# Performance work log

Hardware: AMD Instinct MI355X
Metric: run time of the kernel (lower is better)

The kernel has to match this reference:

```python
import jax, jax.numpy as jnp
import numpy as np

K = 512
U = 2
TEMP_BERN = 0.67
TEMP_CAT = 0.67
EULER = 0.5772156649015329
EPS = 1e-8
UEPS = 1e-6


def setup_inputs() -> dict:
    key = jax.random.key(0)
    ks = jax.random.split(key, 3)
    B, D = 16384, 1024
    inputs = jax.random.normal(ks[0], (B, D), jnp.float32)
    # glorot-normal-ish init for mW
    mW = jax.random.normal(ks[1], (D, K * U), jnp.float32) * jnp.sqrt(2.0 / (D + K * U))
    sW = jnp.full((D, K * U), -5.0, jnp.float32)
    conc1 = jnp.full((K,), 2.0, jnp.float32)
    conc0 = jnp.full((K,), 0.5453, jnp.float32)
    t_pi = jax.random.uniform(ks[2], (D, K), jnp.float32, 4.0, 5.0)
    biases = jnp.full((K * U,), 0.1, jnp.float32)
    return {"inputs": inputs, "mW": mW, "sW": sW, "conc1": conc1,
            "conc0": conc0, "t_pi": t_pi, "biases": biases}


def _uniform(k, shape):
    return jax.random.uniform(k, shape, jnp.float32, UEPS, 1.0 - UEPS)


def reference(inputs, mW, sW, conc1, conc0, t_pi, biases):
    rk = jax.random.split(jax.random.key(42), 4)

    # --- reparameterized weights W = mW + eps * softplus(sW) ---
    sW_sp = jax.nn.softplus(sW)
    eps = jax.lax.stop_gradient(jax.random.normal(rk[0], mW.shape, jnp.float32))
    W = mW + eps * sW_sp
    kl_weights = -0.5 * jnp.mean(2.0 * sW_sp - jnp.square(mW) - jnp.square(sW_sp) + 1.0)
    layer_loss = kl_weights / 60000.0

    # --- IBP: relaxed Bernoulli sample of t_pi ([D, K]) ---
    u = _uniform(rk[1], t_pi.shape)
    logistic = jnp.log(u) - jnp.log1p(-u)
    z_sample = jax.nn.sigmoid((t_pi + logistic) / TEMP_BERN)  # bin_concrete_sample
    z = jnp.tile(z_sample, (1, U))  # [D, K*U], column order u*K+k (as in TF code)

    # Kumaraswamy stick-breaking prior: cumprod along axis 0 (TF default)
    a_sp = jax.nn.softplus(conc1)  # [K]
    b_sp = jax.nn.softplus(conc0)  # [K]
    uk = _uniform(rk[2], t_pi.shape)
    q_u = jnp.power(1.0 - jnp.power(uk, 1.0 / b_sp), 1.0 / a_sp)  # kumaraswamy_sample
    prior_pi = jnp.cumprod(q_u, axis=0)
    q = jax.nn.sigmoid(t_pi)
    kl_z = jnp.sum(q * (jnp.log(q + EPS) - jnp.log(prior_pi + EPS)))

    # KL(Kumaraswamy(a,b) || Beta(1,1)); (beta-1) series term vanishes
    kl_sticks = jnp.sum(((a_sp - 1.0) / a_sp) * (-EULER - jax.scipy.special.digamma(b_sp) - 1.0 / b_sp)
                        + jnp.log(a_sp * b_sp + EPS) - (b_sp - 1.0) / b_sp)
    layer_loss = layer_loss + kl_sticks + kl_z

    W = z * W
    out = inputs @ W + biases  # [B, K*U]

    # --- LWTA activation via Gumbel-softmax over U competitors ---
    logits = out.reshape(-1, K, U)  # [B, K, U]
    g = -jnp.log(-jnp.log(_uniform(rk[3], logits.shape)))
    xi = jax.nn.softmax((logits + g) / TEMP_CAT, axis=-1)  # concrete_sample
    out_act = (logits * xi).reshape(out.shape)
    q_xi = jax.nn.softmax(logits, axis=-1)
    kl_xi = jnp.mean(jnp.sum(q_xi * (jnp.log(q_xi + EPS) - jnp.log(1.0 / U)), axis=1))
    layer_loss = layer_loss + kl_xi

    return out_act, layer_loss
```

## Files before the change

kernel.cpp:

```cpp
#include <hip/hip_runtime.h>
#include <stdint.h>
#include <math.h>

#define B_N   16384
#define D_N   1024
#define K_N   512
#define KU_N  1024
#define EPS_F 1e-8f
#define TEMP  0.67f
#define EULERC 0.5772156649015329f

#define HEPS  524288
#define HU    262144
#define HG    8388608

typedef uint32_t u32;
typedef __attribute__((ext_vector_type(4))) float f32x4;
typedef __attribute__((ext_vector_type(4))) unsigned int u32x4;
typedef __attribute__((ext_vector_type(8))) __bf16 bf16x8;

#define TF_ROT(x, r) (((x) << (r)) | ((x) >> (32 - (r))))

__host__ __device__ static inline void threefry2x32(u32 k0, u32 k1,
                                                    u32 x0, u32 x1,
                                                    u32* o0, u32* o1) {
  u32 ks2 = k0 ^ k1 ^ 0x1BD11BDAu;
  x0 += k0; x1 += k1;
  x0 += x1; x1 = TF_ROT(x1, 13); x1 ^= x0;
  x0 += x1; x1 = TF_ROT(x1, 15); x1 ^= x0;
  x0 += x1; x1 = TF_ROT(x1, 26); x1 ^= x0;
  x0 += x1; x1 = TF_ROT(x1, 6);  x1 ^= x0;
  x0 += k1; x1 += ks2 + 1u;
  x0 += x1; x1 = TF_ROT(x1, 17); x1 ^= x0;
  x0 += x1; x1 = TF_ROT(x1, 29); x1 ^= x0;
  x0 += x1; x1 = TF_ROT(x1, 16); x1 ^= x0;
  x0 += x1; x1 = TF_ROT(x1, 24); x1 ^= x0;
  x0 += ks2; x1 += k0 + 2u;
  x0 += x1; x1 = TF_ROT(x1, 13); x1 ^= x0;
  x0 += x1; x1 = TF_ROT(x1, 15); x1 ^= x0;
  x0 += x1; x1 = TF_ROT(x1, 26); x1 ^= x0;
  x0 += x1; x1 = TF_ROT(x1, 6);  x1 ^= x0;
  x0 += k0; x1 += k1 + 3u;
  x0 += x1; x1 = TF_ROT(x1, 17); x1 ^= x0;
  x0 += x1; x1 = TF_ROT(x1, 29); x1 ^= x0;
  x0 += x1; x1 = TF_ROT(x1, 16); x1 ^= x0;
  x0 += x1; x1 = TF_ROT(x1, 24); x1 ^= x0;
  x0 += k1; x1 += ks2 + 4u;
  x0 += x1; x1 = TF_ROT(x1, 13); x1 ^= x0;
  x0 += x1; x1 = TF_ROT(x1, 15); x1 ^= x0;
  x0 += x1; x1 = TF_ROT(x1, 26); x1 ^= x0;
  x0 += x1; x1 = TF_ROT(x1, 6);  x1 ^= x0;
  x0 += ks2; x1 += k0 + 5u;
  *o0 = x0; *o1 = x1;
}

__device__ static inline float bits_to_u01(u32 b) {
  u32 f = (b >> 9) | 0x3f800000u;
  return __uint_as_float(f) - 1.0f;
}
__device__ static inline float unif_f(u32 b, float lo, float hi) {
  float f = bits_to_u01(b);
  return fmaxf(lo, f * (hi - lo) + lo);
}
__device__ static inline float erfinv_f(float x) {
  float w = -log1pf(-x * x);
  float p;
  if (w < 5.f) {
    w -= 2.5f;
    p = 2.81022636e-08f;
    p = fmaf(p, w, 3.43273939e-07f);
    p = fmaf(p, w, -3.5233877e-06f);
    p = fmaf(p, w, -4.39150654e-06f);
    p = fmaf(p, w, 0.00021858087f);
    p = fmaf(p, w, -0.00125372503f);
    p = fmaf(p, w, -0.00417768164f);
    p = fmaf(p, w, 0.246640727f);
    p = fmaf(p, w, 1.50140941f);
  } else {
    w = sqrtf(w) - 3.f;
    p = -0.000200214257f;
    p = fmaf(p, w, 0.000100950558f);
    p = fmaf(p, w, 0.00134934322f);
    p = fmaf(p, w, -0.00367342844f);
    p = fmaf(p, w, 0.00573950773f);
    p = fmaf(p, w, -0.0076224613f);
    p = fmaf(p, w, 0.00943887047f);
    p = fmaf(p, w, 1.00167406f);
    p = fmaf(p, w, 2.83297682f);
  }
  return p * x;
}
__device__ static inline float softplus_f(float x) {
  return fmaxf(x, 0.f) + log1pf(expf(-fabsf(x)));
}
__device__ static inline float rcp_f(float x) { return __builtin_amdgcn_rcpf(x); }
__device__ static inline float sigmoid_fast(float x) {
  return rcp_f(1.f + __expf(-x));
}
__device__ static inline float digamma_f(float x) {
  float r = 0.f;
  while (x < 6.f) { r -= 1.f / x; x += 1.f; }
  float inv = 1.f / x, inv2 = inv * inv;
  return r + logf(x) - 0.5f * inv
       - inv2 * (1.f / 12.f - inv2 * (1.f / 120.f - inv2 * (1.f / 252.f)));
}
__device__ static inline unsigned short f2bf_rne(float x) {
  u32 u = __float_as_uint(x);
  u32 r = (u + 0x7fffu + ((u >> 16) & 1u)) >> 16;
  return (unsigned short)r;
}
__device__ static inline u32 cvt_pk_bf16(float lo, float hi) {
  u32 r;
  asm("v_cvt_pk_bf16_f32 %0, %1, %2" : "=v"(r) : "v"(lo), "v"(hi));
  return r;
}
__device__ static inline void gload_lds16(const void* g, void* l) {
  __builtin_amdgcn_global_load_lds(
      (const __attribute__((address_space(1))) u32*)g,
      (__attribute__((address_space(3))) u32*)l, 16, 0, 0);
}

__device__ static inline float block_sum(float v) {
  __shared__ float sm[16];
  int lane = threadIdx.x & 63;
  int wid = threadIdx.x >> 6;
  #pragma unroll
  for (int o = 32; o > 0; o >>= 1) v += __shfl_down(v, o, 64);
  if (lane == 0) sm[wid] = v;
  __syncthreads();
  float s = 0.f;
  if (threadIdx.x == 0) {
    int nw = (blockDim.x + 63) >> 6;
    s = sm[0];
    for (int w = 1; w < nw; ++w) s += sm[w];
  }
  return s;
}

__global__ void k_init(const float* __restrict__ conc1,
                       const float* __restrict__ conc0,
                       float* __restrict__ invA, float* __restrict__ invB,
                       float* gacc) {
  int k = threadIdx.x;
  float a = softplus_f(conc1[k]);
  float b = softplus_f(conc0[k]);
  invA[k] = 1.f / a;
  invB[k] = 1.f / b;
  float s = ((a - 1.f) / a) * (-EULERC - digamma_f(b) - 1.f / b)
          + logf(a * b + EPS_F) - (b - 1.f) / b;
  float t = block_sum(s);
  if (threadIdx.x == 0) { gacc[0] = 0.f; gacc[1] = t; gacc[2] = 0.f; }
}

__global__ __launch_bounds__(256) void k_klz_a(const float* __restrict__ invA,
                                               const float* __restrict__ invB,
                                               float* __restrict__ P,
                                               u32 qk0, u32 qk1) {
  int idx = blockIdx.x * 256 + threadIdx.x;
  int c = idx >> 9, k = idx & (K_N - 1);
  float iA = invA[k], iB = invB[k];
  float p = 1.f;
  int d0 = c << 4;
  for (int d = d0; d < d0 + 16; ++d) {
    int n = (d << 9) + k;
    u32 x0 = (n < HU) ? (u32)n : (u32)(n - HU);
    u32 o0, o1;
    threefry2x32(qk0, qk1, x0, x0 + HU, &o0, &o1);
    u32 bits = (n < HU) ? o0 : o1;
    float u = unif_f(bits, 1e-6f, 1.f - 1e-6f);
    p *= powf(1.f - powf(u, iB), iA);
  }
  P[idx] = p;
}

__global__ __launch_bounds__(256) void k_klz_b(const float* __restrict__ t_pi,
                                               const float* __restrict__ invA,
                                               const float* __restrict__ invB,
                                               const float* __restrict__ P,
                                               float* gacc,
                                               u32 qk0, u32 qk1) {
  int idx = blockIdx.x * 256 + threadIdx.x;
  int c = idx >> 9, k = idx & (K_N - 1);
  float iA = invA[k], iB = invB[k];
  float prior = 1.f;
  for (int c2 = 0; c2 < c; ++c2) prior *= P[(c2 << 9) + k];
  float s = 0.f;
  int d0 = c << 4;
  for (int d = d0; d < d0 + 16; ++d) {
    int n = (d << 9) + k;
    u32 x0 = (n < HU) ? (u32)n : (u32)(n - HU);
    u32 o0, o1;
    threefry2x32(qk0, qk1, x0, x0 + HU, &o0, &o1);
    u32 bits = (n < HU) ? o0 : o1;
    float u = unif_f(bits, 1e-6f, 1.f - 1e-6f);
    prior *= powf(1.f - powf(u, iB), iA);
    float q = sigmoid_fast(t_pi[n]);
    s += q * (__logf(q + EPS_F) - __logf(prior + EPS_F));
  }
  float t = block_sum(s);
  if (threadIdx.x == 0) atomicAdd(&gacc[1], t);
}

__global__ __launch_bounds__(256) void k_wbuildT(const float* __restrict__ mW,
                                                 const float* __restrict__ sW,
                                                 const float* __restrict__ t_pi,
                                                 unsigned short* __restrict__ WzT,
                                                 float* __restrict__ gacc,
                                                 u32 ek0, u32 ek1,
                                                 u32 uk0, u32 uk1) {
  __shared__ unsigned short tile[64][65];
  int dt = (int)blockIdx.x >> 4;
  int jt = (int)blockIdx.x & 15;
  int d0 = dt << 6, j0 = jt << 6;
  int tj = threadIdx.x & 63;
  int tr = threadIdx.x >> 6;
  int j = j0 + tj;
  int kk = j & (K_N - 1);
  bool lowD = (dt < 8);
  float klw = 0.f;
  #pragma unroll 4
  for (int rr = 0; rr < 16; ++rr) {
    int dl = (rr << 2) + tr;
    int d = d0 + dl;
    int n = (d << 10) + j;
    u32 x0 = lowD ? (u32)n : (u32)(n - HEPS);
    u32 o0, o1;
    threefry2x32(ek0, ek1, x0, x0 + HEPS, &o0, &o1);
    u32 ebits = lowD ? o0 : o1;
    int nz = (d << 9) + kk;
    u32 zx0 = lowD ? (u32)nz : (u32)(nz - HU);
    u32 z0, z1;
    threefry2x32(uk0, uk1, zx0, zx0 + HU, &z0, &z1);
    u32 zbits = lowD ? z0 : z1;
    float u = unif_f(zbits, 1e-6f, 1.f - 1e-6f);
    float logistic = __logf(u) - log1pf(-u);
    float z = sigmoid_fast((t_pi[nz] + logistic) * (1.f / TEMP));
    float un = unif_f(ebits, -0.99999994f, 1.0f);
    float epsn = 1.41421356f * erfinv_f(un);
    float m = mW[n], sp = softplus_f(sW[n]);
    tile[tj][dl] = f2bf_rne(z * (m + epsn * sp));
    klw += 2.f * sp - m * m - sp * sp + 1.f;
  }
  __syncthreads();
  #pragma unroll 4
  for (int rr = 0; rr < 16; ++rr) {
    int jl = (rr << 2) + tr;
    WzT[(size_t)(j0 + jl) * D_N + d0 + tj] = tile[jl][tj];
  }
  float t = block_sum(klw);
  if (threadIdx.x == 0) atomicAdd(&gacc[0], t);
}

#define TBM 256
#define TBN 256
#define TBK 64

__global__ __launch_bounds__(512, 2) void k_gemm(const float* __restrict__ A,
                                                 const unsigned short* __restrict__ Bt,
                                                 const float* __restrict__ bias,
                                                 float* __restrict__ C) {
  __shared__ __align__(16) unsigned short As[2][TBM * TBK];
  __shared__ __align__(16) unsigned short Bs[2][TBN * TBK];

  int f = (int)blockIdx.x;
  int wk = (f & 7) * 32 + (f >> 3);
  const int brow = (wk >> 2) * TBM;
  const int bcol = (wk & 3) * TBN;

  const int tid = threadIdx.x;
  const int lane = tid & 63;
  const int w = tid >> 6;

  const int ar = tid >> 1;
  const float* gA = A + (size_t)(brow + ar) * D_N + ((tid & 1) << 5);
  const int cb = (tid & 1) << 2;
  int aoff[4];
  #pragma unroll
  for (int i = 0; i < 4; ++i)
    aoff[i] = (ar << 7) + (((cb + i) ^ (ar & 7)) << 4);

  const int bcl = tid >> 3;
  const unsigned short* gB = Bt + (size_t)(bcol + bcl) * D_N
                           + (((tid & 7) ^ (bcl & 7)) << 3);
  const int bdst = (w << 10);

  f32x4 acc[8][4];
  #pragma unroll
  for (int m = 0; m < 8; ++m)
    #pragma unroll
    for (int n = 0; n < 4; ++n) acc[m][n] = (f32x4){0.f, 0.f, 0.f, 0.f};

  const int wrow = (w >> 2) << 7;
  const int wcol = (w & 3) << 6;
  const int fr = lane & 15;
  const int kg = lane >> 4;

  f32x4 av[8];

  #pragma unroll
  for (int j = 0; j < 8; ++j) av[j] = *(const f32x4*)(gA + (j << 2));
  #pragma unroll
  for (int q = 0; q < 4; ++q)
    gload_lds16(gB + (size_t)(q * 64) * D_N, (char*)Bs[0] + q * 8192 + bdst);
  __builtin_amdgcn_sched_barrier(0);
  #pragma unroll
  for (int i = 0; i < 4; ++i) {
    u32x4 p;
    p.x = cvt_pk_bf16(av[2 * i].x, av[2 * i].y);
    p.y = cvt_pk_bf16(av[2 * i].z, av[2 * i].w);
    p.z = cvt_pk_bf16(av[2 * i + 1].x, av[2 * i + 1].y);
    p.w = cvt_pk_bf16(av[2 * i + 1].z, av[2 * i + 1].w);
    *(u32x4*)((char*)As[0] + aoff[i]) = p;
  }
  #pragma unroll
  for (int j = 0; j < 8; ++j) av[j] = *(const f32x4*)(gA + TBK + (j << 2));
  asm volatile("s_waitcnt vmcnt(8) lgkmcnt(0)" ::: "memory");
  __builtin_amdgcn_s_barrier();

  for (int t = 0; t < 15; ++t) {
    const int cur = t & 1;
    char* curA = (char*)As + (cur << 15);
    char* curB = (char*)Bs + (cur << 15);
    char* altA = (char*)As + ((cur ^ 1) << 15);
    char* altB = (char*)Bs + ((cur ^ 1) << 15);

    {
      const unsigned short* gBn = gB + ((t + 1) << 6);
      #pragma unroll
      for (int q = 0; q < 4; ++q)
        gload_lds16(gBn + (size_t)(q * 64) * D_N, altB + q * 8192 + bdst);
    }
    __builtin_amdgcn_sched_barrier(0);

    __builtin_amdgcn_s_setprio(1);
    #pragma unroll
    for (int h = 0; h < 2; ++h) {
      bf16x8 af[8];
      #pragma unroll
      for (int m = 0; m < 8; ++m) {
        int row = wrow + m * 16 + fr;
        af[m] = *(const bf16x8*)(curA + (row << 7) + ((((h << 2) + kg) ^ (row & 7)) << 4));
      }
      #pragma unroll
      for (int n = 0; n < 4; ++n) {
        int col = wcol + n * 16 + fr;
        bf16x8 bf = *(const bf16x8*)(curB + (col << 7) + ((((h << 2) + kg) ^ (col & 7)) << 4));
        #pragma unroll
        for (int m = 0; m < 8; ++m)
          acc[m][n] = __builtin_amdgcn_mfma_f32_16x16x32_bf16(af[m], bf, acc[m][n], 0, 0, 0);
      }
    }
    __builtin_amdgcn_s_setprio(0);

    #pragma unroll
    for (int i = 0; i < 4; ++i) {
      u32x4 p;
      p.x = cvt_pk_bf16(av[2 * i].x, av[2 * i].y);
      p.y = cvt_pk_bf16(av[2 * i].z, av[2 * i].w);
      p.z = cvt_pk_bf16(av[2 * i + 1].x, av[2 * i + 1].y);
      p.w = cvt_pk_bf16(av[2 * i + 1].z, av[2 * i + 1].w);
      *(u32x4*)(altA + aoff[i]) = p;
    }
    if (t < 14) {
      const float* g = gA + ((t + 2) << 6);
      #pragma unroll
      for (int j = 0; j < 8; ++j) av[j] = *(const f32x4*)(g + (j << 2));
    }

    asm volatile("s_waitcnt vmcnt(8) lgkmcnt(0)" ::: "memory");
    __builtin_amdgcn_s_barrier();
  }

  asm volatile("s_waitcnt vmcnt(0)" ::: "memory");
  __builtin_amdgcn_s_barrier();
  {
    char* curA = (char*)As + (1 << 15);
    char* curB = (char*)Bs + (1 << 15);
    #pragma unroll
    for (int h = 0; h < 2; ++h) {
      bf16x8 af[8];
      #pragma unroll
      for (int m = 0; m < 8; ++m) {
        int row = wrow + m * 16 + fr;
        af[m] = *(const bf16x8*)(curA + (row << 7) + ((((h << 2) + kg) ^ (row & 7)) << 4));
      }
      #pragma unroll
      for (int n = 0; n < 4; ++n) {
        int col = wcol + n * 16 + fr;
        bf16x8 bf = *(const bf16x8*)(curB + (col << 7) + ((((h << 2) + kg) ^ (col & 7)) << 4));
        #pragma unroll
        for (int m = 0; m < 8; ++m)
          acc[m][n] = __builtin_amdgcn_mfma_f32_16x16x32_bf16(af[m], bf, acc[m][n], 0, 0, 0);
      }
    }
  }

  #pragma unroll
  for (int n = 0; n < 4; ++n) {
    int col = bcol + wcol + n * 16 + fr;
    float bv = bias[col];
    #pragma unroll
    for (int m = 0; m < 8; ++m) {
      int rowb = brow + wrow + m * 16 + (kg << 2);
      C[(size_t)(rowb + 0) * KU_N + col] = acc[m][n].x + bv;
      C[(size_t)(rowb + 1) * KU_N + col] = acc[m][n].y + bv;
      C[(size_t)(rowb + 2) * KU_N + col] = acc[m][n].z + bv;
      C[(size_t)(rowb + 3) * KU_N + col] = acc[m][n].w + bv;
    }
  }
}

__device__ static inline float lwta_pair(float v0, float v1, u32 ba, u32 bb,
                                         float* o0, float* o1) {
  float u0 = unif_f(ba, 1e-6f, 1.f - 1e-6f);
  float u1 = unif_f(bb, 1e-6f, 1.f - 1e-6f);
  float g0 = -__logf(-__logf(u0));
  float g1 = -__logf(-__logf(u1));
  const float it = 1.f / TEMP;
  float d = ((v1 + g1) - (v0 + g0)) * it;
  float xi0 = rcp_f(1.f + __expf(d));
  float xi1 = 1.f - xi0;
  *o0 = v0 * xi0;
  *o1 = v1 * xi1;
  float qd = v1 - v0;
  float q0 = rcp_f(1.f + __expf(qd));
  float q1 = 1.f - q0;
  const float LOG2F = 0.6931471805599453f;
  return q0 * (__logf(q0 + EPS_F) + LOG2F) + q1 * (__logf(q1 + EPS_F) + LOG2F);
}

__global__ __launch_bounds__(256) void k_epi(float* __restrict__ C,
                                             float* __restrict__ partial,
                                             u32 gk0, u32 gk1) {
  int idx = blockIdx.x * 256 + threadIdx.x;
  int b = idx >> 9;
  int c2 = (idx & 511) << 1;
  size_t p0 = (size_t)b * KU_N + c2;
  size_t p1 = p0 + (size_t)8192 * KU_N;
  float2 r0 = *(const float2*)&C[p0];
  float2 r1 = *(const float2*)&C[p1];
  u32 m = ((u32)b << 10) | (u32)c2;
  u32 x0a, x1a, x0b, x1b;
  threefry2x32(gk0, gk1, m,      m + HG,      &x0a, &x1a);
  threefry2x32(gk0, gk1, m + 1u, m + 1u + HG, &x0b, &x1b);
  float2 w0, w1;
  float kl = lwta_pair(r0.x, r0.y, x0a, x0b, &w0.x, &w0.y)
           + lwta_pair(r1.x, r1.y, x1a, x1b, &w1.x, &w1.y);
  *(float2*)&C[p0] = w0;
  *(float2*)&C[p1] = w1;
  float t = block_sum(kl);
  if (threadIdx.x == 0) partial[blockIdx.x] = t;
}

#define NPART 16384
__global__ __launch_bounds__(256) void k_final(const float* __restrict__ gacc,
                                               const float* __restrict__ partial,
                                               float* __restrict__ out_loss) {
  float s = 0.f;
  for (int i = threadIdx.x; i < NPART; i += 256) s += partial[i];
  float t = block_sum(s);
  if (threadIdx.x == 0) {
    float kl_weights = -0.5f * (gacc[0] * (1.f / 1048576.f));
    out_loss[0] = kl_weights / 60000.f + gacc[1] + t * (1.f / 32768.f);
  }
}

extern "C" void kernel_launch(void* const* d_in, const int* in_sizes, int n_in,
                              void* d_out, int out_size, void* d_ws, size_t ws_size,
                              hipStream_t stream) {
  (void)in_sizes; (void)n_in; (void)out_size; (void)ws_size;
  const float* inputs = (const float*)d_in[0];
  const float* mW     = (const float*)d_in[1];
  const float* sW     = (const float*)d_in[2];
  const float* conc1  = (const float*)d_in[3];
  const float* conc0  = (const float*)d_in[4];
  const float* t_pi   = (const float*)d_in[5];
  const float* biases = (const float*)d_in[6];
  float* out = (float*)d_out;

  u32 a[4], b[4];
  for (int i = 0; i < 4; ++i)
    threefry2x32(0u, 42u, (u32)i, (u32)(i + 4), &a[i], &b[i]);
  u32 e_k0 = a[0], e_k1 = a[1];
  u32 u_k0 = a[2], u_k1 = a[3];
  u32 q_k0 = b[0], q_k1 = b[1];
  u32 g_k0 = b[2], g_k1 = b[3];

  char* wsb = (char*)d_ws;
  unsigned short* WzT = (unsigned short*)wsb;
  float* P       = (float*)(wsb + (2u << 20));
  float* invA    = (float*)(wsb + (2u << 20) + (128u << 10));
  float* invB    = (float*)(wsb + (2u << 20) + (130u << 10));
  float* gacc    = (float*)(wsb + (2u << 20) + (132u << 10));
  float* partial = (float*)(wsb + (2u << 20) + (136u << 10));

  hipLaunchKernelGGL(k_init, dim3(1), dim3(512), 0, stream,
                     conc1, conc0, invA, invB, gacc);
  hipLaunchKernelGGL(k_klz_a, dim3(128), dim3(256), 0, stream,
                     invA, invB, P, q_k0, q_k1);
  hipLaunchKernelGGL(k_klz_b, dim3(128), dim3(256), 0, stream,
                     t_pi, invA, invB, P, gacc, q_k0, q_k1);
  hipLaunchKernelGGL(k_wbuildT, dim3(256), dim3(256), 0, stream,
                     mW, sW, t_pi, WzT, gacc, e_k0, e_k1, u_k0, u_k1);
  hipLaunchKernelGGL(k_gemm, dim3(256), dim3(512), 0, stream,
                     inputs, WzT, biases, out);
  hipLaunchKernelGGL(k_epi, dim3(NPART), dim3(256), 0, stream,
                     out, partial, g_k0, g_k1);
  hipLaunchKernelGGL(k_final, dim3(1), dim3(256), 0, stream,
                     gacc, partial, out + 16777216);
}
```

Before: 189.4 us.

## Split GEMM k-step into two barrier-fenced halves and drop init kernel

The GEMM main loop now splits each K tile into two halves. Each half issues half of the next B tile loads and its A fragment reads, then hits a workgroup barrier before its MFMA block, so global loads, A conversion and MFMA work interleave more finely across waves. Separately, the k_init kernel and the global atomics are removed: stick-breaking KL is computed in k_final, inverse concentrations are recomputed in each KLZ kernel, and per-block partials are written and reduced in k_final. This saves one launch and the atomic contention, but adds barriers inside the GEMM loop and makes k_final do a little more work.

```diff
diff --git a/kernel.cpp b/kernel.cpp
--- a/kernel.cpp
+++ b/kernel.cpp
@@ -137,28 +137,14 @@
   return s;
 }
 
-__global__ void k_init(const float* __restrict__ conc1,
-                       const float* __restrict__ conc0,
-                       float* __restrict__ invA, float* __restrict__ invB,
-                       float* gacc) {
-  int k = threadIdx.x;
-  float a = softplus_f(conc1[k]);
-  float b = softplus_f(conc0[k]);
-  invA[k] = 1.f / a;
-  invB[k] = 1.f / b;
-  float s = ((a - 1.f) / a) * (-EULERC - digamma_f(b) - 1.f / b)
-          + logf(a * b + EPS_F) - (b - 1.f) / b;
-  float t = block_sum(s);
-  if (threadIdx.x == 0) { gacc[0] = 0.f; gacc[1] = t; gacc[2] = 0.f; }
-}
-
-__global__ __launch_bounds__(256) void k_klz_a(const float* __restrict__ invA,
-                                               const float* __restrict__ invB,
+__global__ __launch_bounds__(256) void k_klz_a(const float* __restrict__ conc1,
+                                               const float* __restrict__ conc0,
                                                float* __restrict__ P,
                                                u32 qk0, u32 qk1) {
   int idx = blockIdx.x * 256 + threadIdx.x;
   int c = idx >> 9, k = idx & (K_N - 1);
-  float iA = invA[k], iB = invB[k];
+  float iA = 1.f / softplus_f(conc1[k]);
+  float iB = 1.f / softplus_f(conc0[k]);
   float p = 1.f;
   int d0 = c << 4;
   for (int d = d0; d < d0 + 16; ++d) {
@@ -174,14 +160,15 @@
 }
 
 __global__ __launch_bounds__(256) void k_klz_b(const float* __restrict__ t_pi,
-                                               const float* __restrict__ invA,
-                                               const float* __restrict__ invB,
+                                               const float* __restrict__ conc1,
+                                               const float* __restrict__ conc0,
                                                const float* __restrict__ P,
-                                               float* gacc,
+                                               float* __restrict__ partialZ,
                                                u32 qk0, u32 qk1) {
   int idx = blockIdx.x * 256 + threadIdx.x;
   int c = idx >> 9, k = idx & (K_N - 1);
-  float iA = invA[k], iB = invB[k];
+  float iA = 1.f / softplus_f(conc1[k]);
+  float iB = 1.f / softplus_f(conc0[k]);
   float prior = 1.f;
   for (int c2 = 0; c2 < c; ++c2) prior *= P[(c2 << 9) + k];
   float s = 0.f;
@@ -198,14 +185,14 @@
     s += q * (__logf(q + EPS_F) - __logf(prior + EPS_F));
   }
   float t = block_sum(s);
-  if (threadIdx.x == 0) atomicAdd(&gacc[1], t);
+  if (threadIdx.x == 0) partialZ[blockIdx.x] = t;
 }
 
 __global__ __launch_bounds__(256) void k_wbuildT(const float* __restrict__ mW,
                                                  const float* __restrict__ sW,
                                                  const float* __restrict__ t_pi,
                                                  unsigned short* __restrict__ WzT,
-                                                 float* __restrict__ gacc,
+                                                 float* __restrict__ partialW,
                                                  u32 ek0, u32 ek1,
                                                  u32 uk0, u32 uk1) {
   __shared__ unsigned short tile[64][65];
@@ -248,7 +235,7 @@
     WzT[(size_t)(j0 + jl) * D_N + d0 + tj] = tile[jl][tj];
   }
   float t = block_sum(klw);
-  if (threadIdx.x == 0) atomicAdd(&gacc[0], t);
+  if (threadIdx.x == 0) partialW[blockIdx.x] = t;
 }
 
 #define TBM 256
@@ -323,35 +310,40 @@
     char* curB = (char*)Bs + (cur << 15);
     char* altA = (char*)As + ((cur ^ 1) << 15);
     char* altB = (char*)Bs + ((cur ^ 1) << 15);
-
-    {
-      const unsigned short* gBn = gB + ((t + 1) << 6);
+    const unsigned short* gBn = gB + ((t + 1) << 6);
+
+    gload_lds16(gBn + (size_t)(0 * 64) * D_N, altB + 0 * 8192 + bdst);
+    gload_lds16(gBn + (size_t)(1 * 64) * D_N, altB + 1 * 8192 + bdst);
+    bf16x8 af0[8];
+    #pragma unroll
+    for (int m = 0; m < 8; ++m) {
+      int row = wrow + m * 16 + fr;
+      af0[m] = *(const bf16x8*)(curA + (row << 7) + ((kg ^ (row & 7)) << 4));
+    }
+    __builtin_amdgcn_sched_barrier(0);
+    __builtin_amdgcn_s_barrier();
+    __builtin_amdgcn_sched_barrier(0);
+    __builtin_amdgcn_s_setprio(1);
+    #pragma unroll
+    for (int n = 0; n < 4; ++n) {
+      int col = wcol + n * 16 + fr;
+      bf16x8 bf = *(const bf16x8*)(curB + (col << 7) + ((kg ^ (col & 7)) << 4));
       #pragma unroll
-      for (int q = 0; q < 4; ++q)
-        gload_lds16(gBn + (size_t)(q * 64) * D_N, altB + q * 8192 + bdst);
-    }
+      for (int m = 0; m < 8; ++m)
+        acc[m][n] = __builtin_amdgcn_mfma_f32_16x16x32_bf16(af0[m], bf, acc[m][n], 0, 0, 0);
+    }
+    __builtin_amdgcn_s_setprio(0);
     __builtin_amdgcn_sched_barrier(0);
-
-    __builtin_amdgcn_s_setprio(1);
-    #pragma unroll
-    for (int h = 0; h < 2; ++h) {
-      bf16x8 af[8];
-      #pragma unroll
-      for (int m = 0; m < 8; ++m) {
-        int row = wrow + m * 16 + fr;
-        af[m] = *(const bf16x8*)(curA + (row << 7) + ((((h << 2) + kg) ^ (row & 7)) << 4));
-      }
-      #pragma unroll
-      for (int n = 0; n < 4; ++n) {
-        int col = wcol + n * 16 + fr;
-        bf16x8 bf = *(const bf16x8*)(curB + (col << 7) + ((((h << 2) + kg) ^ (col & 7)) << 4));
-        #pragma unroll
-        for (int m = 0; m < 8; ++m)
-          acc[m][n] = __builtin_amdgcn_mfma_f32_16x16x32_bf16(af[m], bf, acc[m][n], 0, 0, 0);
-      }
-    }
-    __builtin_amdgcn_s_setprio(0);
-
+    __builtin_amdgcn_s_barrier();
+
+    gload_lds16(gBn + (size_t)(2 * 64) * D_N, altB + 2 * 8192 + bdst);
+    gload_lds16(gBn + (size_t)(3 * 64) * D_N, altB + 3 * 8192 + bdst);
+    bf16x8 af1[8];
+    #pragma unroll
+    for (int m = 0; m < 8; ++m) {
+      int row = wrow + m * 16 + fr;
+      af1[m] = *(const bf16x8*)(curA + (row << 7) + (((4 + kg) ^ (row & 7)) << 4));
+    }
     #pragma unroll
     for (int i = 0; i < 4; ++i) {
       u32x4 p;
@@ -366,7 +358,19 @@
       #pragma unroll
       for (int j = 0; j < 8; ++j) av[j] = *(const f32x4*)(g + (j << 2));
     }
-
+    __builtin_amdgcn_sched_barrier(0);
+    __builtin_amdgcn_s_barrier();
+    __builtin_amdgcn_sched_barrier(0);
+    __builtin_amdgcn_s_setprio(1);
+    #pragma unroll
+    for (int n = 0; n < 4; ++n) {
+      int col = wcol + n * 16 + fr;
+      bf16x8 bf = *(const bf16x8*)(curB + (col << 7) + (((4 + kg) ^ (col & 7)) << 4));
+      #pragma unroll
+      for (int m = 0; m < 8; ++m)
+        acc[m][n] = __builtin_amdgcn_mfma_f32_16x16x32_bf16(af1[m], bf, acc[m][n], 0, 0, 0);
+    }
+    __builtin_amdgcn_s_setprio(0);
     asm volatile("s_waitcnt vmcnt(8) lgkmcnt(0)" ::: "memory");
     __builtin_amdgcn_s_barrier();
   }
@@ -453,16 +457,25 @@
 }
 
 #define NPART 16384
-__global__ __launch_bounds__(256) void k_final(const float* __restrict__ gacc,
+__global__ __launch_bounds__(512) void k_final(const float* __restrict__ conc1,
+                                               const float* __restrict__ conc0,
                                                const float* __restrict__ partial,
+                                               const float* __restrict__ partialW,
+                                               const float* __restrict__ partialZ,
                                                float* __restrict__ out_loss) {
-  float s = 0.f;
-  for (int i = threadIdx.x; i < NPART; i += 256) s += partial[i];
-  float t = block_sum(s);
-  if (threadIdx.x == 0) {
-    float kl_weights = -0.5f * (gacc[0] * (1.f / 1048576.f));
-    out_loss[0] = kl_weights / 60000.f + gacc[1] + t * (1.f / 32768.f);
-  }
+  int tid = threadIdx.x;
+  float a = softplus_f(conc1[tid]);
+  float b = softplus_f(conc0[tid]);
+  float stick = ((a - 1.f) / a) * (-EULERC - digamma_f(b) - 1.f / b)
+              + logf(a * b + EPS_F) - (b - 1.f) / b;
+  float s_xi = 0.f;
+  for (int i = tid; i < NPART; i += 512) s_xi += partial[i];
+  float s_w = (tid < 256) ? partialW[tid] : 0.f;
+  float s_z = (tid < 128) ? partialZ[tid] : 0.f;
+  float v = stick + s_z + s_xi * (1.f / 32768.f)
+          + s_w * (-0.5f / 1048576.f / 60000.f);
+  float t = block_sum(v);
+  if (tid == 0) out_loss[0] = t;
 }
 
 extern "C" void kernel_launch(void* const* d_in, const int* in_sizes, int n_in,
@@ -488,24 +501,21 @@
 
   char* wsb = (char*)d_ws;
   unsigned short* WzT = (unsigned short*)wsb;
-  float* P       = (float*)(wsb + (2u << 20));
-  float* invA    = (float*)(wsb + (2u << 20) + (128u << 10));
-  float* invB    = (float*)(wsb + (2u << 20) + (130u << 10));
-  float* gacc    = (float*)(wsb + (2u << 20) + (132u << 10));
-  float* partial = (float*)(wsb + (2u << 20) + (136u << 10));
-
-  hipLaunchKernelGGL(k_init, dim3(1), dim3(512), 0, stream,
-                     conc1, conc0, invA, invB, gacc);
+  float* P        = (float*)(wsb + (2u << 20));
+  float* partial  = (float*)(wsb + (2u << 20) + (128u << 10));
+  float* partialW = (float*)(wsb + (2u << 20) + (192u << 10));
+  float* partialZ = (float*)(wsb + (2u << 20) + (193u << 10));
+
   hipLaunchKernelGGL(k_klz_a, dim3(128), dim3(256), 0, stream,
-                     invA, invB, P, q_k0, q_k1);
+                     conc1, conc0, P, q_k0, q_k1);
   hipLaunchKernelGGL(k_klz_b, dim3(128), dim3(256), 0, stream,
-                     t_pi, invA, invB, P, gacc, q_k0, q_k1);
+                     t_pi, conc1, conc0, P, partialZ, q_k0, q_k1);
   hipLaunchKernelGGL(k_wbuildT, dim3(256), dim3(256), 0, stream,
-                     mW, sW, t_pi, WzT, gacc, e_k0, e_k1, u_k0, u_k1);
+                     mW, sW, t_pi, WzT, partialW, e_k0, e_k1, u_k0, u_k1);
   hipLaunchKernelGGL(k_gemm, dim3(256), dim3(512), 0, stream,
                      inputs, WzT, biases, out);
   hipLaunchKernelGGL(k_epi, dim3(NPART), dim3(256), 0, stream,
                      out, partial, g_k0, g_k1);
-  hipLaunchKernelGGL(k_final, dim3(1), dim3(256), 0, stream,
-                     gacc, partial, out + 16777216);
-}
+  hipLaunchKernelGGL(k_final, dim3(1), dim3(512), 0, stream,
+                     conc1, conc0, partial, partialW, partialZ, out + 16777216);
+}
```

Measured after the change: 188.7 us. Within noise of the previous version (-0.4%).
